# Optimization experiments

Hardware: AMD Instinct MI355X
Metric: run time of the kernel (lower is better)

The kernel has to match this reference:

```python
import jax, jax.numpy as jnp
import numpy as np

WS = 7          # window size
NH = 6          # heads per block
H = 112
W = 112
SHIFTS = (0, 3, 0, 3)  # alternating W-MSA / SW-MSA over depths=[2,2]


def _ln(x, g, b, eps=1e-5):
    m = x.mean(-1, keepdims=True)
    v = x.var(-1, keepdims=True)
    return (x - m) / jnp.sqrt(v + eps) * g + b


def _rel_idx():
    coords = np.stack(np.meshgrid(np.arange(WS), np.arange(WS), indexing='ij'))
    flat = coords.reshape(2, -1)
    rel = (flat[:, :, None] - flat[:, None, :]).transpose(1, 2, 0)
    rel[:, :, 0] += WS - 1
    rel[:, :, 1] += WS - 1
    rel[:, :, 0] *= 2 * WS - 1
    return rel.sum(-1)  # (49, 49) indices into the (2*WS-1)^2 bias table


def _attn_mask(shift):
    # standard Swin shifted-window attention mask, (nW, 49, 49)
    img = np.zeros((H, W))
    cnt = 0
    for hs in (slice(0, -WS), slice(-WS, -shift), slice(-shift, None)):
        for ws_ in (slice(0, -WS), slice(-WS, -shift), slice(-shift, None)):
            img[hs, ws_] = cnt
            cnt += 1
    win = img.reshape(H // WS, WS, W // WS, WS).transpose(0, 2, 1, 3).reshape(-1, WS * WS)
    m = win[:, None, :] - win[:, :, None]
    return np.where(m != 0, -100.0, 0.0).astype(np.float32)


def _win_part(x):  # (B,H,W,C) -> (B*nW, 49, C)
    B, _, _, C = x.shape
    x = x.reshape(B, H // WS, WS, W // WS, WS, C).transpose(0, 1, 3, 2, 4, 5)
    return x.reshape(-1, WS * WS, C)


def _win_rev(w, B, C):  # (B*nW, 49, C) -> (B,H,W,C)
    x = w.reshape(B, H // WS, W // WS, WS, WS, C).transpose(0, 1, 3, 2, 4, 5)
    return x.reshape(B, H, W, C)


def setup_inputs() -> dict:
    key = jax.random.key(0)
    ks = jax.random.split(key, 8)
    C, NB, B = 180, 4, 2
    f = lambda k, s: jax.random.normal(k, s, dtype=jnp.float32) * 0.02
    return {
        'x': jax.random.normal(ks[0], (B, C, H, W), dtype=jnp.float32),
        'pe_g': jnp.ones((C,), jnp.float32), 'pe_b': jnp.zeros((C,), jnp.float32),
        'ln1_g': jnp.ones((NB, C), jnp.float32), 'ln1_b': jnp.zeros((NB, C), jnp.float32),
        'qkv_w': f(ks[1], (NB, C, 3 * C)), 'qkv_b': jnp.zeros((NB, 3 * C), jnp.float32),
        'proj_w': f(ks[2], (NB, C, C)), 'proj_b': jnp.zeros((NB, C), jnp.float32),
        'ln2_g': jnp.ones((NB, C), jnp.float32), 'ln2_b': jnp.zeros((NB, C), jnp.float32),
        'fc1_w': f(ks[3], (NB, C, 4 * C)), 'fc1_b': jnp.zeros((NB, 4 * C), jnp.float32),
        'fc2_w': f(ks[4], (NB, 4 * C, C)), 'fc2_b': jnp.zeros((NB, C), jnp.float32),
        'rpb': f(ks[5], (NB, (2 * WS - 1) ** 2, NH)),
        'fn_g': jnp.ones((C,), jnp.float32), 'fn_b': jnp.zeros((C,), jnp.float32),
    }


def reference(x, pe_g, pe_b, ln1_g, ln1_b, qkv_w, qkv_b, proj_w, proj_b,
              ln2_g, ln2_b, fc1_w, fc1_b, fc2_w, fc2_b, rpb, fn_g, fn_b):
    B, C = x.shape[0], x.shape[1]
    dh = C // NH
    scale = dh ** -0.5
    rel_idx = jnp.asarray(_rel_idx())
    mask3 = jnp.asarray(_attn_mask(3))
    nW = (H // WS) * (W // WS)

    t = x.reshape(B, C, H * W).transpose(0, 2, 1)  # (B, L, C) tokens
    t = _ln(t, pe_g, pe_b)                          # patch_norm
    for i, shift in enumerate(SHIFTS):
        h = _ln(t, ln1_g[i], ln1_b[i]).reshape(B, H, W, C)
        if shift:
            h = jnp.roll(h, (-shift, -shift), axis=(1, 2))
        w = _win_part(h)                                            # (B*nW, 49, C)
        qkv = (w @ qkv_w[i] + qkv_b[i]).reshape(-1, WS * WS, 3, NH, dh)
        qkv = qkv.transpose(2, 0, 3, 1, 4)                          # (3, B*nW, NH, 49, dh)
        q, k, v = qkv[0] * scale, qkv[1], qkv[2]
        attn = jnp.einsum('bhid,bhjd->bhij', q, k)
        bias = rpb[i][rel_idx].transpose(2, 0, 1)                   # (NH, 49, 49)
        attn = attn + bias[None]
        if shift:
            attn = attn.reshape(B, nW, NH, WS * WS, WS * WS) + mask3[None, :, None]
            attn = attn.reshape(-1, NH, WS * WS, WS * WS)
        attn = jax.nn.softmax(attn, axis=-1)
        o = jnp.einsum('bhij,bhjd->bhid', attn, v)
        o = o.transpose(0, 2, 1, 3).reshape(-1, WS * WS, C)
        o = o @ proj_w[i] + proj_b[i]
        h = _win_rev(o, B, C)
        if shift:
            h = jnp.roll(h, (shift, shift), axis=(1, 2))
        t = t + h.reshape(B, H * W, C)                              # residual (drop_path=id at eval)
        m = _ln(t, ln2_g[i], ln2_b[i])
        m = jax.nn.gelu(m @ fc1_w[i] + fc1_b[i], approximate=False)
        t = t + (m @ fc2_w[i] + fc2_b[i])
    t = _ln(t, fn_g, fn_b)
    return t.reshape(B, H, W, C).transpose(0, 3, 1, 2)  # SwinBlock permute back to BCHW
```

## Files before the change

### kernel.cpp

```cpp
#include <hip/hip_runtime.h>
#include <hip/hip_bf16.h>
#include <cmath>

typedef __hip_bfloat16 bf16;
typedef short short8 __attribute__((ext_vector_type(8)));
typedef float f32x4  __attribute__((ext_vector_type(4)));

#define Cc    180
#define KP1   192
#define KP2   736
#define Hh    112
#define Wwid  112
#define Ltok  12544
#define Bsz   2
#define TOK   25088
#define WSz   7
#define NHd   6
#define DHd   30
#define NWIN  256
#define P49   49

__device__ __forceinline__ float LD(const void* p, size_t i, int f) {
    if (f) return ((const float*)p)[i];
    return (float)((const bf16*)p)[i];
}
__device__ __forceinline__ void ST(void* p, size_t i, int f, float v) {
    if (f) ((float*)p)[i] = v;
    else   ((bf16*)p)[i] = (bf16)v;
}

__device__ __forceinline__ short bh(float x) { bf16 t = (bf16)x; return *(short*)&t; }
__device__ __forceinline__ short8 cvt8(float4 a, float4 b) {
    short8 o;
    o[0] = bh(a.x); o[1] = bh(a.y); o[2] = bh(a.z); o[3] = bh(a.w);
    o[4] = bh(b.x); o[5] = bh(b.y); o[6] = bh(b.z); o[7] = bh(b.w);
    return o;
}

__device__ __forceinline__ float wred(float v) {
    v += __shfl_xor(v, 1);
    v += __shfl_xor(v, 2);
    v += __shfl_xor(v, 4);
    v += __shfl_xor(v, 8);
    v += __shfl_xor(v, 16);
    v += __shfl_xor(v, 32);
    return v;
}

__global__ void k_detect(const unsigned short* __restrict__ xb, int* __restrict__ flag) {
    __shared__ int s;
    if (threadIdx.x == 0) s = 0;
    __syncthreads();
    int bad = 0;
    for (int i = threadIdx.x; i < 2048; i += 256) {
        int e = (xb[i] >> 7) & 0xFF;
        if (e >= 0xC8) bad = 1;
    }
    if (bad) atomicOr(&s, 1);
    __syncthreads();
    if (threadIdx.x == 0) flag[0] = s;
}

__global__ __launch_bounds__(256) void k_tr(const void* __restrict__ src, size_t woff,
                                            bf16* __restrict__ dst,
                                            int K, int N, int Kp, int Npad,
                                            const int* __restrict__ dflag) {
    int f = *dflag;
    int idx = blockIdx.x * 256 + threadIdx.x;
    if (idx >= Npad * Kp) return;
    int n = idx / Kp, k = idx % Kp;
    float v = (n < N && k < K) ? LD(src, woff + (size_t)k * N + n, f) : 0.f;
    dst[idx] = (bf16)v;
}

__global__ __launch_bounds__(256) void k_trq(const void* __restrict__ src, size_t woff,
                                             bf16* __restrict__ dst,
                                             const int* __restrict__ dflag) {
    int f = *dflag;
    int idx = blockIdx.x * 256 + threadIdx.x;
    if (idx >= 576 * KP1) return;
    int n = idx / KP1, k = idx % KP1;
    int sec = n / 192, rm = n % 192, hd = rm >> 5, d = rm & 31;
    float v = (d < 30 && k < 180) ? LD(src, woff + (size_t)k * 540 + sec * 180 + hd * 30 + d, f) : 0.f;
    dst[idx] = (bf16)v;
}

__global__ __launch_bounds__(256) void k_bias(const void* __restrict__ rpb,
                                              float* __restrict__ BT,
                                              const int* __restrict__ dflag) {
    int f = *dflag;
    int idx = blockIdx.x * 256 + threadIdx.x;
    if (idx >= 4 * NHd * 4096) return;
    int blk = idx / (NHd * 4096);
    int rem0 = idx % (NHd * 4096);
    int hd = rem0 >> 12, rem = rem0 & 4095;
    int i = rem >> 6, j = rem & 63;
    float v;
    if (i < 49 && j < 49) {
        int rel = (i / 7 - j / 7 + 6) * 13 + (i % 7 - j % 7 + 6);
        v = LD(rpb, (size_t)blk * 169 * NHd + (size_t)rel * NHd + hd, f);
    } else {
        v = -1.0e9f;
    }
    BT[idx] = v;
}

__global__ __launch_bounds__(256) void k_patchnorm(const void* __restrict__ x,
                                                   const void* __restrict__ g,
                                                   const void* __restrict__ b,
                                                   float* __restrict__ T,
                                                   const int* __restrict__ dflag) {
    int f = *dflag;
    int tokid = blockIdx.x * 4 + (threadIdx.x >> 6);
    int lane  = threadIdx.x & 63;
    int bb = tokid / Ltok, ll = tokid % Ltok;
    size_t base = (size_t)bb * Cc * Ltok + ll;
    float v0 = LD(x, base + (size_t)lane * Ltok, f);
    float v1 = LD(x, base + (size_t)(lane + 64) * Ltok, f);
    float v2 = (lane < 52) ? LD(x, base + (size_t)(lane + 128) * Ltok, f) : 0.f;
    float s  = wred(v0 + v1 + v2);
    float sq = wred(v0 * v0 + v1 * v1 + v2 * v2);
    float mean = s * (1.f / 180.f);
    float var  = sq * (1.f / 180.f) - mean * mean;
    float rstd = rsqrtf(var + 1e-5f);
    float* tp = T + (size_t)tokid * Cc;
    tp[lane]      = (v0 - mean) * rstd * LD(g, lane, f)      + LD(b, lane, f);
    tp[lane + 64] = (v1 - mean) * rstd * LD(g, lane + 64, f) + LD(b, lane + 64, f);
    if (lane < 52)
        tp[lane + 128] = (v2 - mean) * rstd * LD(g, lane + 128, f) + LD(b, lane + 128, f);
}

__global__ __launch_bounds__(256) void k_ln(const float* __restrict__ T,
                                            const void* __restrict__ g,
                                            const void* __restrict__ b,
                                            bf16* __restrict__ D,
                                            int windowed, int shift, int goff,
                                            const int* __restrict__ dflag) {
    int f = *dflag;
    int r    = blockIdx.x * 4 + (threadIdx.x >> 6);
    int lane = threadIdx.x & 63;
    int src;
    if (windowed) {
        int bb  = r / (NWIN * P49);
        int rem = r % (NWIN * P49);
        int wi = rem / P49, p = rem % P49;
        int wy = wi >> 4, wx = wi & 15;
        int py = p / 7, px = p % 7;
        int gh = (wy * 7 + py + shift) % Hh;
        int gw = (wx * 7 + px + shift) % Wwid;
        src = bb * Ltok + gh * Wwid + gw;
    } else {
        src = r;
    }
    const float* tp = T + (size_t)src * Cc;
    float v0 = tp[lane];
    float v1 = tp[lane + 64];
    float v2 = (lane < 52) ? tp[lane + 128] : 0.f;
    float s  = wred(v0 + v1 + v2);
    float sq = wred(v0 * v0 + v1 * v1 + v2 * v2);
    float mean = s * (1.f / 180.f);
    float var  = sq * (1.f / 180.f) - mean * mean;
    float rstd = rsqrtf(var + 1e-5f);
    bf16* dp = D + (size_t)r * KP1;
    dp[lane]      = (bf16)((v0 - mean) * rstd * LD(g, goff + lane, f)      + LD(b, goff + lane, f));
    dp[lane + 64] = (bf16)((v1 - mean) * rstd * LD(g, goff + lane + 64, f) + LD(b, goff + lane + 64, f));
    if (lane < 52)
        dp[lane + 128] = (bf16)((v2 - mean) * rstd * LD(g, goff + lane + 128, f) + LD(b, goff + lane + 128, f));
    else
        dp[lane + 128] = (bf16)0.f;
}

__global__ __launch_bounds__(256) void k_final(const float* __restrict__ T,
                                               const void* __restrict__ g,
                                               const void* __restrict__ b,
                                               void* __restrict__ out,
                                               const int* __restrict__ dflag) {
    int f = *dflag;
    int tokid = blockIdx.x * 4 + (threadIdx.x >> 6);
    int lane  = threadIdx.x & 63;
    int bb = tokid / Ltok, ll = tokid % Ltok;
    const float* tp = T + (size_t)tokid * Cc;
    float v0 = tp[lane];
    float v1 = tp[lane + 64];
    float v2 = (lane < 52) ? tp[lane + 128] : 0.f;
    float s  = wred(v0 + v1 + v2);
    float sq = wred(v0 * v0 + v1 * v1 + v2 * v2);
    float mean = s * (1.f / 180.f);
    float var  = sq * (1.f / 180.f) - mean * mean;
    float rstd = rsqrtf(var + 1e-5f);
    size_t base = (size_t)bb * Cc * Ltok + ll;
    ST(out, base + (size_t)lane * Ltok,        f, (v0 - mean) * rstd * LD(g, lane, f)      + LD(b, lane, f));
    ST(out, base + (size_t)(lane + 64) * Ltok, f, (v1 - mean) * rstd * LD(g, lane + 64, f) + LD(b, lane + 64, f));
    if (lane < 52)
        ST(out, base + (size_t)(lane + 128) * Ltok, f,
           (v2 - mean) * rstd * LD(g, lane + 128, f) + LD(b, lane + 128, f));
}

template <int EPI>
__global__ __launch_bounds__(256) void k_mgemm(const bf16* __restrict__ A,
                                               const bf16* __restrict__ Wt,
                                               const void* __restrict__ bias,
                                               size_t boff, int Nbias,
                                               bf16* __restrict__ OutB, int ldOut, int Nstore,
                                               float* __restrict__ OutF,
                                               int Kp, int shift, int rowoff,
                                               const int* __restrict__ dflag) {
    __shared__ __align__(16) char SM[64 * 72 * 4];
    short* Als = (short*)SM;
    short* Bls = (short*)(SM + 8192);
    float* Els = (float*)SM;
    int tid = threadIdx.x, lane = tid & 63, w = tid >> 6;
    int wr = w >> 1, wc = w & 1;
    int q = lane >> 4, c = lane & 15;
    int m0 = blockIdx.y * 128, n0 = blockIdx.x * 64;
    f32x4 acc[4][2] = {};

    int rowA0 = m0 + (tid >> 6) * 16 + (tid & 15);
    int rowW  = n0 + (tid >> 6) * 16 + (tid & 15);
    int koff  = ((tid >> 4) & 3) * 8;
    const bf16* pa0 = A + (size_t)rowA0 * Kp + koff;
    const bf16* pa1 = A + (size_t)(rowA0 + 64) * Kp + koff;
    const bf16* pw  = Wt + (size_t)rowW * Kp + koff;
    ulonglong2 rA0 = *(const ulonglong2*)pa0;
    ulonglong2 rA1 = *(const ulonglong2*)pa1;
    ulonglong2 rW  = *(const ulonglong2*)pw;

    for (int k0 = 0; k0 < Kp; k0 += 32) {
        *(ulonglong2*)&Als[tid * 8]         = rA0;
        *(ulonglong2*)&Als[(tid + 256) * 8] = rA1;
        *(ulonglong2*)&Bls[tid * 8]         = rW;
        __syncthreads();
        if (k0 + 32 < Kp) {
            rA0 = *(const ulonglong2*)(pa0 + k0 + 32);
            rA1 = *(const ulonglong2*)(pa1 + k0 + 32);
            rW  = *(const ulonglong2*)(pw  + k0 + 32);
        }
        short8 b0 = *(const short8*)&Bls[((wc * 2 + 0) * 64 + lane) * 8];
        short8 b1 = *(const short8*)&Bls[((wc * 2 + 1) * 64 + lane) * 8];
#pragma unroll
        for (int mt = 0; mt < 4; ++mt) {
            short8 a = *(const short8*)&Als[((wr * 4 + mt) * 64 + lane) * 8];
            acc[mt][0] = __builtin_amdgcn_mfma_f32_16x16x32_bf16(a, b0, acc[mt][0], 0, 0, 0);
            acc[mt][1] = __builtin_amdgcn_mfma_f32_16x16x32_bf16(a, b1, acc[mt][1], 0, 0, 0);
        }
        __syncthreads();
    }

    int f = *dflag;
#pragma unroll
    for (int Ph = 0; Ph < 2; ++Ph) {
        if (Ph) __syncthreads();
        if (wr == Ph) {
#pragma unroll
            for (int mt = 0; mt < 4; ++mt)
#pragma unroll
                for (int nt = 0; nt < 2; ++nt)
#pragma unroll
                    for (int r = 0; r < 4; ++r) {
                        int rl = mt * 16 + q * 4 + r;
                        int cl = (wc * 2 + nt) * 16 + c;
                        int col = n0 + cl;
                        float val = acc[mt][nt][r];
                        if (EPI == 4) {
                            int sec = col / 192, rm = col % 192;
                            int hd = rm >> 5, d = rm & 31;
                            if (d < 30) val += LD(bias, boff + sec * 180 + hd * 30 + d, f);
                            if (sec == 0) val *= 0.18257418583505536f;
                        } else if (EPI == 1) {
                            if (col < Nbias) val += LD(bias, boff + col, f);
                            val = 0.5f * val * (1.f + erff(val * 0.70710678118654752f));
                        } else {
                            if (col < Nstore) val += LD(bias, boff + col, f);
                        }
                        Els[rl * 72 + cl] = val;
                    }
        }
        __syncthreads();
        if (EPI == 1 || EPI == 4) {
#pragma unroll
            for (int it = 0; it < 2; ++it) {
                int ri = it * 256 + tid;
                int row = ri >> 3, c8 = ri & 7;
                int gcol = n0 + c8 * 8;
                if (gcol < Nstore) {
                    float4 v0 = *(float4*)&Els[row * 72 + c8 * 8];
                    float4 v1 = *(float4*)&Els[row * 72 + c8 * 8 + 4];
                    short8 o = cvt8(v0, v1);
                    *(ulonglong2*)(OutB + (size_t)(m0 + Ph * 64 + row) * ldOut + gcol) =
                        *(ulonglong2*)&o;
                }
            }
        } else {
#pragma unroll
            for (int it = 0; it < 4; ++it) {
                int ri = it * 256 + tid;
                int row = ri >> 4, c4 = ri & 15;
                int col = n0 + c4 * 4;
                if (col < Nstore) {
                    int grow = rowoff + m0 + Ph * 64 + row;
                    int tgt = grow;
                    if (EPI == 3) {
                        int bb  = grow / (NWIN * P49);
                        int rem = grow % (NWIN * P49);
                        int wi = rem / P49, p = rem % P49;
                        int wy = wi >> 4, wx = wi & 15;
                        int py = p / 7, px = p % 7;
                        int gh = (wy * 7 + py + shift) % Hh;
                        int gw = (wx * 7 + px + shift) % Wwid;
                        tgt = bb * Ltok + gh * Wwid + gw;
                    }
                    float4* tp = (float4*)(OutF + (size_t)tgt * Cc + col);
                    float4 t = *tp;
                    float4 e = *(float4*)&Els[row * 72 + c4 * 4];
                    t.x += e.x; t.y += e.y; t.z += e.z; t.w += e.w;
                    *tp = t;
                }
            }
        }
    }
}

__device__ __forceinline__ int regionOf(int g, int shift) {
    return (g < Hh - WSz) ? 0 : ((g < Hh - shift) ? 1 : 2);
}

__global__ __launch_bounds__(64) void k_mattn(const bf16* __restrict__ QKV,
                                              const bf16* __restrict__ Vt_unused,
                                              const float* __restrict__ BT,
                                              bf16* __restrict__ Ow,
                                              int shift, int w0) {
    __shared__ __align__(16) bf16 P[64 * 72];
    __shared__ __align__(16) bf16 Vl[32 * 72];
    int lane = threadIdx.x;
    int lw = blockIdx.x / NHd, hd = blockIdx.x % NHd;
    int r0 = lw * P49;
    int q = lane >> 4, c = lane & 15;

    const bf16* qb = QKV + (size_t)(r0 + c) * 576 + hd * 32 + q * 8;
    short8 qf[4], kf[4];
#pragma unroll
    for (int t = 0; t < 4; ++t) {
        qf[t] = *(const short8*)(qb + (size_t)t * 16 * 576);
        kf[t] = *(const short8*)(qb + 192 + (size_t)t * 16 * 576);
    }
    for (int t = lane; t < 32 * 15; t += 64) {
        int d = t / 15, p = 49 + t % 15;
        Vl[d * 72 + p] = (bf16)0.f;
    }
    for (int t = lane; t < P49 * 4; t += 64) {
        int p = t >> 2, ch = t & 3;
        ulonglong2 v = *(const ulonglong2*)(QKV + (size_t)(r0 + p) * 576 + 384 + hd * 32 + ch * 8);
        bf16* vv = (bf16*)&v;
#pragma unroll
        for (int j = 0; j < 8; ++j) Vl[(ch * 8 + j) * 72 + p] = vv[j];
    }

    f32x4 zero = {0.f, 0.f, 0.f, 0.f};
    f32x4 S[4][4];
#pragma unroll
    for (int mt = 0; mt < 4; ++mt)
#pragma unroll
        for (int nt = 0; nt < 4; ++nt)
            S[mt][nt] = __builtin_amdgcn_mfma_f32_16x16x32_bf16(qf[mt], kf[nt], zero, 0, 0, 0);

    const float* bt = BT + hd * 4096;
    int wi = (w0 + lw) & (NWIN - 1);
    int wy = wi >> 4, wx = wi & 15;
    int lj[4], li[4][4];
    if (shift) {
#pragma unroll
        for (int nt = 0; nt < 4; ++nt) {
            int j = nt * 16 + c;
            lj[nt] = (j < 49) ? regionOf(wy * 7 + j / 7, shift) * 3 + regionOf(wx * 7 + j % 7, shift) : -1;
        }
#pragma unroll
        for (int mt = 0; mt < 4; ++mt)
#pragma unroll
            for (int r = 0; r < 4; ++r) {
                int i = mt * 16 + q * 4 + r;
                li[mt][r] = (i < 49) ? regionOf(wy * 7 + i / 7, shift) * 3 + regionOf(wx * 7 + i % 7, shift) : -2;
            }
    }
    float rmax[4][4];
#pragma unroll
    for (int mt = 0; mt < 4; ++mt)
#pragma unroll
        for (int r = 0; r < 4; ++r) rmax[mt][r] = -3.0e38f;
#pragma unroll
    for (int mt = 0; mt < 4; ++mt)
#pragma unroll
        for (int nt = 0; nt < 4; ++nt)
#pragma unroll
            for (int r = 0; r < 4; ++r) {
                int i = mt * 16 + q * 4 + r, j = nt * 16 + c;
                float v = S[mt][nt][r] + bt[i * 64 + j];
                if (shift && li[mt][r] != lj[nt]) v -= 100.f;
                S[mt][nt][r] = v;
                rmax[mt][r] = fmaxf(rmax[mt][r], v);
            }
#pragma unroll
    for (int mt = 0; mt < 4; ++mt)
#pragma unroll
        for (int r = 0; r < 4; ++r) {
            float m = rmax[mt][r];
            m = fmaxf(m, __shfl_xor(m, 1));
            m = fmaxf(m, __shfl_xor(m, 2));
            m = fmaxf(m, __shfl_xor(m, 4));
            m = fmaxf(m, __shfl_xor(m, 8));
            rmax[mt][r] = m;
        }
    float rsum[4][4] = {};
#pragma unroll
    for (int mt = 0; mt < 4; ++mt)
#pragma unroll
        for (int nt = 0; nt < 4; ++nt)
#pragma unroll
            for (int r = 0; r < 4; ++r) {
                float e = __expf(S[mt][nt][r] - rmax[mt][r]);
                S[mt][nt][r] = e;
                rsum[mt][r] += e;
            }
#pragma unroll
    for (int mt = 0; mt < 4; ++mt)
#pragma unroll
        for (int r = 0; r < 4; ++r) {
            float s = rsum[mt][r];
            s += __shfl_xor(s, 1);
            s += __shfl_xor(s, 2);
            s += __shfl_xor(s, 4);
            s += __shfl_xor(s, 8);
            rsum[mt][r] = 1.f / s;
        }
#pragma unroll
    for (int mt = 0; mt < 4; ++mt)
#pragma unroll
        for (int nt = 0; nt < 4; ++nt)
#pragma unroll
            for (int r = 0; r < 4; ++r)
                P[(mt * 16 + q * 4 + r) * 72 + nt * 16 + c] = (bf16)(S[mt][nt][r] * rsum[mt][r]);
    __syncthreads();

    f32x4 O[4][2] = {};
#pragma unroll
    for (int ks = 0; ks < 2; ++ks) {
        short8 vf0 = *(const short8*)&Vl[(0  + c) * 72 + ks * 32 + q * 8];
        short8 vf1 = *(const short8*)&Vl[(16 + c) * 72 + ks * 32 + q * 8];
#pragma unroll
        for (int mt = 0; mt < 4; ++mt) {
            short8 pf = *(const short8*)&P[(mt * 16 + c) * 72 + ks * 32 + q * 8];
            O[mt][0] = __builtin_amdgcn_mfma_f32_16x16x32_bf16(pf, vf0, O[mt][0], 0, 0, 0);
            O[mt][1] = __builtin_amdgcn_mfma_f32_16x16x32_bf16(pf, vf1, O[mt][1], 0, 0, 0);
        }
    }
    int r0g = (w0 + lw) * P49;
#pragma unroll
    for (int mt = 0; mt < 4; ++mt)
#pragma unroll
        for (int nt = 0; nt < 2; ++nt)
#pragma unroll
            for (int r = 0; r < 4; ++r) {
                int i = mt * 16 + q * 4 + r, d = nt * 16 + c;
                if (i < 49 && d < 30)
                    Ow[(size_t)(r0g + i) * KP1 + hd * 30 + d] = (bf16)O[mt][nt][r];
            }
    if (hd == 0) {
        for (int idx = lane; idx < P49 * 12; idx += 64) {
            int p = idx / 12, cp = 180 + idx % 12;
            Ow[(size_t)(r0g + p) * KP1 + cp] = (bf16)0.f;
        }
    }
}

extern "C" void kernel_launch(void* const* d_in, const int* in_sizes, int n_in,
                              void* d_out, int out_size, void* d_ws, size_t ws_size,
                              hipStream_t stream) {
    const void* x      = d_in[0];
    const void* pe_g   = d_in[1];
    const void* pe_b   = d_in[2];
    const void* ln1_g  = d_in[3];
    const void* ln1_b  = d_in[4];
    const void* qkv_w  = d_in[5];
    const void* qkv_b  = d_in[6];
    const void* proj_w = d_in[7];
    const void* proj_b = d_in[8];
    const void* ln2_g  = d_in[9];
    const void* ln2_b  = d_in[10];
    const void* fc1_w  = d_in[11];
    const void* fc1_b  = d_in[12];
    const void* fc2_w  = d_in[13];
    const void* fc2_b  = d_in[14];
    const void* rpb    = d_in[15];
    const void* fn_g   = d_in[16];
    const void* fn_b   = d_in[17];

    const size_t wtQ = (size_t)576 * KP1, wtP = (size_t)192 * KP1;
    const size_t wtF1 = (size_t)768 * KP1, wtF2 = (size_t)192 * KP2;
    const size_t wtPerBlk = wtQ + wtP + wtF1 + wtF2;

    int*   dflag = (int*)d_ws;
    float* T     = (float*)((char*)d_ws + 256);
    bf16*  Abuf  = (bf16*)(T + (size_t)TOK * Cc);
    bf16*  Wts   = Abuf + (size_t)TOK * KP1;
    float* BT4   = (float*)(Wts + 4 * wtPerBlk);
    bf16*  Bbuf  = (bf16*)(BT4 + 4 * NHd * 4096);
    size_t fixed = (size_t)((char*)Bbuf - (char*)d_ws);

    int c = 1;
    while (c < 4 && fixed + (size_t)(TOK / c) * KP2 * 2 > ws_size) c <<= 1;
    int CM = TOK / c;
    int CW = (Bsz * NWIN) / c;

    dim3 b256(256);
    k_detect<<<1, b256, 0, stream>>>((const unsigned short*)x, dflag);

    for (int i = 0; i < 4; ++i) {
        bf16* wq  = Wts + i * wtPerBlk;
        bf16* wp  = wq + wtQ;
        bf16* wf1 = wp + wtP;
        bf16* wf2 = wf1 + wtF1;
        k_trq<<<(int)((wtQ + 255) / 256), b256, 0, stream>>>(qkv_w, (size_t)i * Cc * 540, wq, dflag);
        k_tr<<<(int)((wtP  + 255) / 256), b256, 0, stream>>>(proj_w, (size_t)i * Cc * Cc,  wp,  180, 180, KP1, 192, dflag);
        k_tr<<<(int)((wtF1 + 255) / 256), b256, 0, stream>>>(fc1_w,  (size_t)i * Cc * 720, wf1, 180, 720, KP1, 768, dflag);
        k_tr<<<(int)((wtF2 + 255) / 256), b256, 0, stream>>>(fc2_w,  (size_t)i * 720 * Cc, wf2, 720, 180, KP2, 192, dflag);
    }
    k_bias<<<(4 * NHd * 4096 + 255) / 256, b256, 0, stream>>>(rpb, BT4, dflag);

    k_patchnorm<<<TOK / 4, b256, 0, stream>>>(x, pe_g, pe_b, T, dflag);

    const int shifts[4] = {0, 3, 0, 3};
    for (int i = 0; i < 4; ++i) {
        int sh = shifts[i];
        bf16* wq  = Wts + i * wtPerBlk;
        bf16* wp  = wq + wtQ;
        bf16* wf1 = wp + wtP;
        bf16* wf2 = wf1 + wtF1;

        k_ln<<<TOK / 4, b256, 0, stream>>>(T, ln1_g, ln1_b, Abuf, 1, sh, i * Cc, dflag);
        for (int j = 0; j < c; ++j) {
            int R0 = j * CM;
            k_mgemm<4><<<dim3(9, CM / 128), b256, 0, stream>>>(
                Abuf + (size_t)R0 * KP1, wq, qkv_b, (size_t)i * 540, 540,
                Bbuf, 576, 576, nullptr, KP1, 0, 0, dflag);
            k_mattn<<<CW * NHd, 64, 0, stream>>>(Bbuf, nullptr, BT4 + i * NHd * 4096,
                                                 Abuf, sh, j * CW);
            k_mgemm<3><<<dim3(3, CM / 128), b256, 0, stream>>>(
                Abuf + (size_t)R0 * KP1, wp, proj_b, (size_t)i * Cc, Cc,
                nullptr, 0, Cc, T, KP1, sh, R0, dflag);
        }
        k_ln<<<TOK / 4, b256, 0, stream>>>(T, ln2_g, ln2_b, Abuf, 0, 0, i * Cc, dflag);
        for (int j = 0; j < c; ++j) {
            int R0 = j * CM;
            k_mgemm<1><<<dim3(12, CM / 128), b256, 0, stream>>>(
                Abuf + (size_t)R0 * KP1, wf1, fc1_b, (size_t)i * 720, 720,
                Bbuf, KP2, KP2, nullptr, KP1, 0, 0, dflag);
            k_mgemm<2><<<dim3(3, CM / 128), b256, 0, stream>>>(
                Bbuf, wf2, fc2_b, (size_t)i * Cc, Cc,
                nullptr, 0, Cc, T, KP2, 0, R0, dflag);
        }
    }

    k_final<<<TOK / 4, b256, 0, stream>>>(T, fn_g, fn_b, d_out, dflag);
}
```

Baseline: 936.0 us.

## Add K=192 GEMM variant holding weights in registers and full A tile in LDS

Adds a specialized GEMM kernel for the K=192 projections (QKV, attention proj, fc1). Each wave keeps its entire weight slice in registers and the block stages the whole 128x192 A tile into padded LDS at once. This replaces the per-32-K loop with its double sync and LDS round-trips. It raises register and LDS use (about 50KB per block, 3 blocks/SM hint), which may limit occupancy. The fc2 GEMM (K=736) keeps the old kernel.

```diff
diff --git a/kernel.cpp b/kernel.cpp
--- a/kernel.cpp
+++ b/kernel.cpp
@@ -19,6 +19,7 @@
 #define DHd   30
 #define NWIN  256
 #define P49   49
+#define LPAD  200
 
 __device__ __forceinline__ float LD(const void* p, size_t i, int f) {
     if (f) return ((const float*)p)[i];
@@ -197,54 +198,57 @@
 }
 
 template <int EPI>
-__global__ __launch_bounds__(256) void k_mgemm(const bf16* __restrict__ A,
-                                               const bf16* __restrict__ Wt,
-                                               const void* __restrict__ bias,
-                                               size_t boff, int Nbias,
-                                               bf16* __restrict__ OutB, int ldOut, int Nstore,
-                                               float* __restrict__ OutF,
-                                               int Kp, int shift, int rowoff,
-                                               const int* __restrict__ dflag) {
-    __shared__ __align__(16) char SM[64 * 72 * 4];
+__global__ __launch_bounds__(256, 3) void k_mgemmL(const bf16* __restrict__ A,
+                                                   const bf16* __restrict__ Wt,
+                                                   const void* __restrict__ bias,
+                                                   size_t boff, int Nbias,
+                                                   bf16* __restrict__ OutB, int ldOut, int Nstore,
+                                                   float* __restrict__ OutF,
+                                                   int shift, int rowoff,
+                                                   const int* __restrict__ dflag) {
+    __shared__ __align__(16) char SM[128 * LPAD * 2];
     short* Als = (short*)SM;
-    short* Bls = (short*)(SM + 8192);
     float* Els = (float*)SM;
     int tid = threadIdx.x, lane = tid & 63, w = tid >> 6;
     int wr = w >> 1, wc = w & 1;
     int q = lane >> 4, c = lane & 15;
     int m0 = blockIdx.y * 128, n0 = blockIdx.x * 64;
+
+    short8 wreg[12];
+    const bf16* wb = Wt + (size_t)(n0 + wc * 32 + c) * 192 + q * 8;
+#pragma unroll
+    for (int ks = 0; ks < 6; ++ks) {
+        wreg[ks * 2 + 0] = *(const short8*)(wb + ks * 32);
+        wreg[ks * 2 + 1] = *(const short8*)(wb + 16 * 192 + ks * 32);
+    }
+
+#pragma unroll
+    for (int rnd = 0; rnd < 2; ++rnd) {
+        ulonglong2 st[6];
+#pragma unroll
+        for (int i = 0; i < 6; ++i) {
+            int g = rnd * 1536 + i * 256 + tid;
+            st[i] = *(const ulonglong2*)(A + (size_t)(m0 + g / 24) * 192 + (g % 24) * 8);
+        }
+#pragma unroll
+        for (int i = 0; i < 6; ++i) {
+            int g = rnd * 1536 + i * 256 + tid;
+            *(ulonglong2*)&Als[(g / 24) * LPAD + (g % 24) * 8] = st[i];
+        }
+    }
+    __syncthreads();
+
     f32x4 acc[4][2] = {};
-
-    int rowA0 = m0 + (tid >> 6) * 16 + (tid & 15);
-    int rowW  = n0 + (tid >> 6) * 16 + (tid & 15);
-    int koff  = ((tid >> 4) & 3) * 8;
-    const bf16* pa0 = A + (size_t)rowA0 * Kp + koff;
-    const bf16* pa1 = A + (size_t)(rowA0 + 64) * Kp + koff;
-    const bf16* pw  = Wt + (size_t)rowW * Kp + koff;
-    ulonglong2 rA0 = *(const ulonglong2*)pa0;
-    ulonglong2 rA1 = *(const ulonglong2*)pa1;
-    ulonglong2 rW  = *(const ulonglong2*)pw;
-
-    for (int k0 = 0; k0 < Kp; k0 += 32) {
-        *(ulonglong2*)&Als[tid * 8]         = rA0;
-        *(ulonglong2*)&Als[(tid + 256) * 8] = rA1;
-        *(ulonglong2*)&Bls[tid * 8]         = rW;
-        __syncthreads();
-        if (k0 + 32 < Kp) {
-            rA0 = *(const ulonglong2*)(pa0 + k0 + 32);
-            rA1 = *(const ulonglong2*)(pa1 + k0 + 32);
-            rW  = *(const ulonglong2*)(pw  + k0 + 32);
-        }
-        short8 b0 = *(const short8*)&Bls[((wc * 2 + 0) * 64 + lane) * 8];
-        short8 b1 = *(const short8*)&Bls[((wc * 2 + 1) * 64 + lane) * 8];
+#pragma unroll
+    for (int ks = 0; ks < 6; ++ks) {
 #pragma unroll
         for (int mt = 0; mt < 4; ++mt) {
-            short8 a = *(const short8*)&Als[((wr * 4 + mt) * 64 + lane) * 8];
-            acc[mt][0] = __builtin_amdgcn_mfma_f32_16x16x32_bf16(a, b0, acc[mt][0], 0, 0, 0);
-            acc[mt][1] = __builtin_amdgcn_mfma_f32_16x16x32_bf16(a, b1, acc[mt][1], 0, 0, 0);
-        }
-        __syncthreads();
-    }
+            short8 a = *(const short8*)&Als[(wr * 64 + mt * 16 + c) * LPAD + ks * 32 + q * 8];
+            acc[mt][0] = __builtin_amdgcn_mfma_f32_16x16x32_bf16(a, wreg[ks * 2 + 0], acc[mt][0], 0, 0, 0);
+            acc[mt][1] = __builtin_amdgcn_mfma_f32_16x16x32_bf16(a, wreg[ks * 2 + 1], acc[mt][1], 0, 0, 0);
+        }
+    }
+    __syncthreads();
 
     int f = *dflag;
 #pragma unroll
@@ -320,6 +324,130 @@
     }
 }
 
+template <int EPI>
+__global__ __launch_bounds__(256) void k_mgemm(const bf16* __restrict__ A,
+                                               const bf16* __restrict__ Wt,
+                                               const void* __restrict__ bias,
+                                               size_t boff, int Nbias,
+                                               bf16* __restrict__ OutB, int ldOut, int Nstore,
+                                               float* __restrict__ OutF,
+                                               int Kp, int shift, int rowoff,
+                                               const int* __restrict__ dflag) {
+    __shared__ __align__(16) char SM[64 * 72 * 4];
+    short* Als = (short*)SM;
+    short* Bls = (short*)(SM + 8192);
+    float* Els = (float*)SM;
+    int tid = threadIdx.x, lane = tid & 63, w = tid >> 6;
+    int wr = w >> 1, wc = w & 1;
+    int q = lane >> 4, c = lane & 15;
+    int m0 = blockIdx.y * 128, n0 = blockIdx.x * 64;
+    f32x4 acc[4][2] = {};
+
+    int rowA0 = m0 + (tid >> 6) * 16 + (tid & 15);
+    int rowW  = n0 + (tid >> 6) * 16 + (tid & 15);
+    int koff  = ((tid >> 4) & 3) * 8;
+    const bf16* pa0 = A + (size_t)rowA0 * Kp + koff;
+    const bf16* pa1 = A + (size_t)(rowA0 + 64) * Kp + koff;
+    const bf16* pw  = Wt + (size_t)rowW * Kp + koff;
+    ulonglong2 rA0 = *(const ulonglong2*)pa0;
+    ulonglong2 rA1 = *(const ulonglong2*)pa1;
+    ulonglong2 rW  = *(const ulonglong2*)pw;
+
+    for (int k0 = 0; k0 < Kp; k0 += 32) {
+        *(ulonglong2*)&Als[tid * 8]         = rA0;
+        *(ulonglong2*)&Als[(tid + 256) * 8] = rA1;
+        *(ulonglong2*)&Bls[tid * 8]         = rW;
+        __syncthreads();
+        if (k0 + 32 < Kp) {
+            rA0 = *(const ulonglong2*)(pa0 + k0 + 32);
+            rA1 = *(const ulonglong2*)(pa1 + k0 + 32);
+            rW  = *(const ulonglong2*)(pw  + k0 + 32);
+        }
+        short8 b0 = *(const short8*)&Bls[((wc * 2 + 0) * 64 + lane) * 8];
+        short8 b1 = *(const short8*)&Bls[((wc * 2 + 1) * 64 + lane) * 8];
+#pragma unroll
+        for (int mt = 0; mt < 4; ++mt) {
+            short8 a = *(const short8*)&Als[((wr * 4 + mt) * 64 + lane) * 8];
+            acc[mt][0] = __builtin_amdgcn_mfma_f32_16x16x32_bf16(a, b0, acc[mt][0], 0, 0, 0);
+            acc[mt][1] = __builtin_amdgcn_mfma_f32_16x16x32_bf16(a, b1, acc[mt][1], 0, 0, 0);
+        }
+        __syncthreads();
+    }
+
+    int f = *dflag;
+#pragma unroll
+    for (int Ph = 0; Ph < 2; ++Ph) {
+        if (Ph) __syncthreads();
+        if (wr == Ph) {
+#pragma unroll
+            for (int mt = 0; mt < 4; ++mt)
+#pragma unroll
+                for (int nt = 0; nt < 2; ++nt)
+#pragma unroll
+                    for (int r = 0; r < 4; ++r) {
+                        int rl = mt * 16 + q * 4 + r;
+                        int cl = (wc * 2 + nt) * 16 + c;
+                        int col = n0 + cl;
+                        float val = acc[mt][nt][r];
+                        if (EPI == 4) {
+                            int sec = col / 192, rm = col % 192;
+                            int hd = rm >> 5, d = rm & 31;
+                            if (d < 30) val += LD(bias, boff + sec * 180 + hd * 30 + d, f);
+                            if (sec == 0) val *= 0.18257418583505536f;
+                        } else if (EPI == 1) {
+                            if (col < Nbias) val += LD(bias, boff + col, f);
+                            val = 0.5f * val * (1.f + erff(val * 0.70710678118654752f));
+                        } else {
+                            if (col < Nstore) val += LD(bias, boff + col, f);
+                        }
+                        Els[rl * 72 + cl] = val;
+                    }
+        }
+        __syncthreads();
+        if (EPI == 1 || EPI == 4) {
+#pragma unroll
+            for (int it = 0; it < 2; ++it) {
+                int ri = it * 256 + tid;
+                int row = ri >> 3, c8 = ri & 7;
+                int gcol = n0 + c8 * 8;
+                if (gcol < Nstore) {
+                    float4 v0 = *(float4*)&Els[row * 72 + c8 * 8];
+                    float4 v1 = *(float4*)&Els[row * 72 + c8 * 8 + 4];
+                    short8 o = cvt8(v0, v1);
+                    *(ulonglong2*)(OutB + (size_t)(m0 + Ph * 64 + row) * ldOut + gcol) =
+                        *(ulonglong2*)&o;
+                }
+            }
+        } else {
+#pragma unroll
+            for (int it = 0; it < 4; ++it) {
+                int ri = it * 256 + tid;
+                int row = ri >> 4, c4 = ri & 15;
+                int col = n0 + c4 * 4;
+                if (col < Nstore) {
+                    int grow = rowoff + m0 + Ph * 64 + row;
+                    int tgt = grow;
+                    if (EPI == 3) {
+                        int bb  = grow / (NWIN * P49);
+                        int rem = grow % (NWIN * P49);
+                        int wi = rem / P49, p = rem % P49;
+                        int wy = wi >> 4, wx = wi & 15;
+                        int py = p / 7, px = p % 7;
+                        int gh = (wy * 7 + py + shift) % Hh;
+                        int gw = (wx * 7 + px + shift) % Wwid;
+                        tgt = bb * Ltok + gh * Wwid + gw;
+                    }
+                    float4* tp = (float4*)(OutF + (size_t)tgt * Cc + col);
+                    float4 t = *tp;
+                    float4 e = *(float4*)&Els[row * 72 + c4 * 4];
+                    t.x += e.x; t.y += e.y; t.z += e.z; t.w += e.w;
+                    *tp = t;
+                }
+            }
+        }
+    }
+}
+
 __device__ __forceinline__ int regionOf(int g, int shift) {
     return (g < Hh - WSz) ? 0 : ((g < Hh - shift) ? 1 : 2);
 }
@@ -538,21 +666,21 @@
         k_ln<<<TOK / 4, b256, 0, stream>>>(T, ln1_g, ln1_b, Abuf, 1, sh, i * Cc, dflag);
         for (int j = 0; j < c; ++j) {
             int R0 = j * CM;
-            k_mgemm<4><<<dim3(9, CM / 128), b256, 0, stream>>>(
+            k_mgemmL<4><<<dim3(9, CM / 128), b256, 0, stream>>>(
                 Abuf + (size_t)R0 * KP1, wq, qkv_b, (size_t)i * 540, 540,
-                Bbuf, 576, 576, nullptr, KP1, 0, 0, dflag);
+                Bbuf, 576, 576, nullptr, 0, 0, dflag);
             k_mattn<<<CW * NHd, 64, 0, stream>>>(Bbuf, nullptr, BT4 + i * NHd * 4096,
                                                  Abuf, sh, j * CW);
-            k_mgemm<3><<<dim3(3, CM / 128), b256, 0, stream>>>(
+            k_mgemmL<3><<<dim3(3, CM / 128), b256, 0, stream>>>(
                 Abuf + (size_t)R0 * KP1, wp, proj_b, (size_t)i * Cc, Cc,
-                nullptr, 0, Cc, T, KP1, sh, R0, dflag);
+                nullptr, 0, Cc, T, sh, R0, dflag);
         }
         k_ln<<<TOK / 4, b256, 0, stream>>>(T, ln2_g, ln2_b, Abuf, 0, 0, i * Cc, dflag);
         for (int j = 0; j < c; ++j) {
             int R0 = j * CM;
-            k_mgemm<1><<<dim3(12, CM / 128), b256, 0, stream>>>(
+            k_mgemmL<1><<<dim3(12, CM / 128), b256, 0, stream>>>(
                 Abuf + (size_t)R0 * KP1, wf1, fc1_b, (size_t)i * 720, 720,
-                Bbuf, KP2, KP2, nullptr, KP1, 0, 0, dflag);
+                Bbuf, KP2, KP2, nullptr, 0, 0, dflag);
             k_mgemm<2><<<dim3(3, CM / 128), b256, 0, stream>>>(
                 Bbuf, wf2, fc2_b, (size_t)i * Cc, Cc,
                 nullptr, 0, Cc, T, KP2, 0, R0, dflag);
```

After: 1.024 ms. 1.09x slower.

## Double-buffer GEMM LDS tiles and remap block grid for XCD locality

Applied to the files above, without the earlier changes.

The GEMM main loop now ping-pongs between two LDS buffers with two register prefetch stages, which removes one of the two barriers per k-step and lets global loads run further ahead of the MFMAs. Blocks are also launched on a flat 1D grid and remapped so that consecutive groups of eight blocks land on different row tiles. The aim is to spread work across the chiplets (XCDs) and improve L2 reuse of the shared weight tile. This adds LDS use, raising it from about 18KB to 24KB, plus extra registers, and launches padded blocks that exit early.

```diff
diff --git a/kernel.cpp b/kernel.cpp
--- a/kernel.cpp
+++ b/kernel.cpp
@@ -204,15 +204,19 @@
                                                bf16* __restrict__ OutB, int ldOut, int Nstore,
                                                float* __restrict__ OutF,
                                                int Kp, int shift, int rowoff,
+                                               int gx, int gy,
                                                const int* __restrict__ dflag) {
-    __shared__ __align__(16) char SM[64 * 72 * 4];
-    short* Als = (short*)SM;
-    short* Bls = (short*)(SM + 8192);
+    __shared__ __align__(16) char SM[24576];
     float* Els = (float*)SM;
+    int flat = blockIdx.x;
+    int X = flat & 7, s = flat >> 3;
+    int bx = s % gx, byi = s / gx;
+    int by = X + 8 * byi;
+    if (by >= gy) return;
     int tid = threadIdx.x, lane = tid & 63, w = tid >> 6;
     int wr = w >> 1, wc = w & 1;
     int q = lane >> 4, c = lane & 15;
-    int m0 = blockIdx.y * 128, n0 = blockIdx.x * 64;
+    int m0 = by * 128, n0 = bx * 64;
     f32x4 acc[4][2] = {};
 
     int rowA0 = m0 + (tid >> 6) * 16 + (tid & 15);
@@ -221,30 +225,43 @@
     const bf16* pa0 = A + (size_t)rowA0 * Kp + koff;
     const bf16* pa1 = A + (size_t)(rowA0 + 64) * Kp + koff;
     const bf16* pw  = Wt + (size_t)rowW * Kp + koff;
-    ulonglong2 rA0 = *(const ulonglong2*)pa0;
-    ulonglong2 rA1 = *(const ulonglong2*)pa1;
-    ulonglong2 rW  = *(const ulonglong2*)pw;
-
-    for (int k0 = 0; k0 < Kp; k0 += 32) {
-        *(ulonglong2*)&Als[tid * 8]         = rA0;
-        *(ulonglong2*)&Als[(tid + 256) * 8] = rA1;
-        *(ulonglong2*)&Bls[tid * 8]         = rW;
-        __syncthreads();
-        if (k0 + 32 < Kp) {
-            rA0 = *(const ulonglong2*)(pa0 + k0 + 32);
-            rA1 = *(const ulonglong2*)(pa1 + k0 + 32);
-            rW  = *(const ulonglong2*)(pw  + k0 + 32);
-        }
-        short8 b0 = *(const short8*)&Bls[((wc * 2 + 0) * 64 + lane) * 8];
-        short8 b1 = *(const short8*)&Bls[((wc * 2 + 1) * 64 + lane) * 8];
-#pragma unroll
-        for (int mt = 0; mt < 4; ++mt) {
-            short8 a = *(const short8*)&Als[((wr * 4 + mt) * 64 + lane) * 8];
-            acc[mt][0] = __builtin_amdgcn_mfma_f32_16x16x32_bf16(a, b0, acc[mt][0], 0, 0, 0);
-            acc[mt][1] = __builtin_amdgcn_mfma_f32_16x16x32_bf16(a, b1, acc[mt][1], 0, 0, 0);
-        }
-        __syncthreads();
-    }
+
+    int nk = Kp >> 5;
+    ulonglong2 sA0[2], sA1[2], sW[2];
+    sA0[0] = *(const ulonglong2*)pa0;
+    sA1[0] = *(const ulonglong2*)pa1;
+    sW[0]  = *(const ulonglong2*)pw;
+    sA0[1] = *(const ulonglong2*)(pa0 + 32);
+    sA1[1] = *(const ulonglong2*)(pa1 + 32);
+    sW[1]  = *(const ulonglong2*)(pw + 32);
+
+    for (int it = 0; it < nk; it += 2) {
+#pragma unroll
+        for (int half = 0; half < 2; ++half) {
+            if (half && it + 1 >= nk) break;
+            short* Als = (short*)(SM + half * 12288);
+            short* Bls = (short*)(SM + half * 12288 + 8192);
+            *(ulonglong2*)&Als[tid * 8]         = sA0[half];
+            *(ulonglong2*)&Als[(tid + 256) * 8] = sA1[half];
+            *(ulonglong2*)&Bls[tid * 8]         = sW[half];
+            int nxt = it + half + 2;
+            if (nxt < nk) {
+                sA0[half] = *(const ulonglong2*)(pa0 + nxt * 32);
+                sA1[half] = *(const ulonglong2*)(pa1 + nxt * 32);
+                sW[half]  = *(const ulonglong2*)(pw  + nxt * 32);
+            }
+            __syncthreads();
+            short8 b0 = *(const short8*)&Bls[((wc * 2 + 0) * 64 + lane) * 8];
+            short8 b1 = *(const short8*)&Bls[((wc * 2 + 1) * 64 + lane) * 8];
+#pragma unroll
+            for (int mt = 0; mt < 4; ++mt) {
+                short8 a = *(const short8*)&Als[((wr * 4 + mt) * 64 + lane) * 8];
+                acc[mt][0] = __builtin_amdgcn_mfma_f32_16x16x32_bf16(a, b0, acc[mt][0], 0, 0, 0);
+                acc[mt][1] = __builtin_amdgcn_mfma_f32_16x16x32_bf16(a, b1, acc[mt][1], 0, 0, 0);
+            }
+        }
+    }
+    __syncthreads();
 
     int f = *dflag;
 #pragma unroll
@@ -509,6 +526,8 @@
     while (c < 4 && fixed + (size_t)(TOK / c) * KP2 * 2 > ws_size) c <<= 1;
     int CM = TOK / c;
     int CW = (Bsz * NWIN) / c;
+    int gy  = CM / 128;
+    int gyp = (gy + 7) & ~7;
 
     dim3 b256(256);
     k_detect<<<1, b256, 0, stream>>>((const unsigned short*)x, dflag);
@@ -538,24 +557,24 @@
         k_ln<<<TOK / 4, b256, 0, stream>>>(T, ln1_g, ln1_b, Abuf, 1, sh, i * Cc, dflag);
         for (int j = 0; j < c; ++j) {
             int R0 = j * CM;
-            k_mgemm<4><<<dim3(9, CM / 128), b256, 0, stream>>>(
+            k_mgemm<4><<<dim3(9 * gyp), b256, 0, stream>>>(
                 Abuf + (size_t)R0 * KP1, wq, qkv_b, (size_t)i * 540, 540,
-                Bbuf, 576, 576, nullptr, KP1, 0, 0, dflag);
+                Bbuf, 576, 576, nullptr, KP1, 0, 0, 9, gy, dflag);
             k_mattn<<<CW * NHd, 64, 0, stream>>>(Bbuf, nullptr, BT4 + i * NHd * 4096,
                                                  Abuf, sh, j * CW);
-            k_mgemm<3><<<dim3(3, CM / 128), b256, 0, stream>>>(
+            k_mgemm<3><<<dim3(3 * gyp), b256, 0, stream>>>(
                 Abuf + (size_t)R0 * KP1, wp, proj_b, (size_t)i * Cc, Cc,
-                nullptr, 0, Cc, T, KP1, sh, R0, dflag);
+                nullptr, 0, Cc, T, KP1, sh, R0, 3, gy, dflag);
         }
         k_ln<<<TOK / 4, b256, 0, stream>>>(T, ln2_g, ln2_b, Abuf, 0, 0, i * Cc, dflag);
         for (int j = 0; j < c; ++j) {
             int R0 = j * CM;
-            k_mgemm<1><<<dim3(12, CM / 128), b256, 0, stream>>>(
+            k_mgemm<1><<<dim3(12 * gyp), b256, 0, stream>>>(
                 Abuf + (size_t)R0 * KP1, wf1, fc1_b, (size_t)i * 720, 720,
-                Bbuf, KP2, KP2, nullptr, KP1, 0, 0, dflag);
-            k_mgemm<2><<<dim3(3, CM / 128), b256, 0, stream>>>(
+                Bbuf, KP2, KP2, nullptr, KP1, 0, 0, 12, gy, dflag);
+            k_mgemm<2><<<dim3(3 * gyp), b256, 0, stream>>>(
                 Bbuf, wf2, fc2_b, (size_t)i * Cc, Cc,
-                nullptr, 0, Cc, T, KP2, 0, R0, dflag);
+                nullptr, 0, Cc, T, KP2, 0, R0, 3, gy, dflag);
         }
     }
 
```

Measured after the change: 1.414 ms. +51.1%, slower.

## Double-buffer GEMM LDS tiles using direct global-to-LDS async loads

Applied to the files above, without the earlier changes.

The MFMA GEMM kernel previously staged each K-slice through registers, with one buffer and a store-then-sync step on every iteration. It now issues 16-byte global_load_lds copies straight into one of two LDS buffers and prefetches the next K-slice while the current one is consumed. This is meant to cut register traffic and overlap memory latency with MFMA work. In exchange, shared memory grows to 24KB, which may lower occupancy, and correctness relies on the barrier waiting for the asynchronous LDS writes.

```diff
diff --git a/kernel.cpp b/kernel.cpp
--- a/kernel.cpp
+++ b/kernel.cpp
@@ -35,6 +35,13 @@
     o[0] = bh(a.x); o[1] = bh(a.y); o[2] = bh(a.z); o[3] = bh(a.w);
     o[4] = bh(b.x); o[5] = bh(b.y); o[6] = bh(b.z); o[7] = bh(b.w);
     return o;
+}
+
+__device__ __forceinline__ void gload16(const bf16* g, void* l) {
+    __builtin_amdgcn_global_load_lds(
+        (const __attribute__((address_space(1))) unsigned int*)g,
+        (__attribute__((address_space(3))) unsigned int*)l,
+        16, 0, 0);
 }
 
 __device__ __forceinline__ float wred(float v) {
@@ -205,9 +212,7 @@
                                                float* __restrict__ OutF,
                                                int Kp, int shift, int rowoff,
                                                const int* __restrict__ dflag) {
-    __shared__ __align__(16) char SM[64 * 72 * 4];
-    short* Als = (short*)SM;
-    short* Bls = (short*)(SM + 8192);
+    __shared__ __align__(16) char SM[24576];
     float* Els = (float*)SM;
     int tid = threadIdx.x, lane = tid & 63, w = tid >> 6;
     int wr = w >> 1, wc = w & 1;
@@ -221,20 +226,22 @@
     const bf16* pa0 = A + (size_t)rowA0 * Kp + koff;
     const bf16* pa1 = A + (size_t)(rowA0 + 64) * Kp + koff;
     const bf16* pw  = Wt + (size_t)rowW * Kp + koff;
-    ulonglong2 rA0 = *(const ulonglong2*)pa0;
-    ulonglong2 rA1 = *(const ulonglong2*)pa1;
-    ulonglong2 rW  = *(const ulonglong2*)pw;
-
-    for (int k0 = 0; k0 < Kp; k0 += 32) {
-        *(ulonglong2*)&Als[tid * 8]         = rA0;
-        *(ulonglong2*)&Als[(tid + 256) * 8] = rA1;
-        *(ulonglong2*)&Bls[tid * 8]         = rW;
-        __syncthreads();
-        if (k0 + 32 < Kp) {
-            rA0 = *(const ulonglong2*)(pa0 + k0 + 32);
-            rA1 = *(const ulonglong2*)(pa1 + k0 + 32);
-            rW  = *(const ulonglong2*)(pw  + k0 + 32);
-        }
+    int nk = Kp >> 5;
+
+#define STAGE(h, kk) do {                                   \
+        char* _b = SM + (h) * 12288;                        \
+        gload16(pa0 + (kk), _b + tid * 16);                 \
+        gload16(pa1 + (kk), _b + 4096 + tid * 16);          \
+        gload16(pw  + (kk), _b + 8192 + tid * 16);          \
+    } while (0)
+
+    STAGE(0, 0);
+    __syncthreads();
+    int cur = 0;
+    for (int it = 0; it < nk; ++it) {
+        if (it + 1 < nk) STAGE(cur ^ 1, (it + 1) * 32);
+        short* Als = (short*)(SM + cur * 12288);
+        short* Bls = (short*)(SM + cur * 12288 + 8192);
         short8 b0 = *(const short8*)&Bls[((wc * 2 + 0) * 64 + lane) * 8];
         short8 b1 = *(const short8*)&Bls[((wc * 2 + 1) * 64 + lane) * 8];
 #pragma unroll
@@ -244,7 +251,9 @@
             acc[mt][1] = __builtin_amdgcn_mfma_f32_16x16x32_bf16(a, b1, acc[mt][1], 0, 0, 0);
         }
         __syncthreads();
-    }
+        cur ^= 1;
+    }
+#undef STAGE
 
     int f = *dflag;
 #pragma unroll
```

After: 935.8 us. Within noise of the previous version (-0.0%).
